# Performance work log

Measured on AMD Instinct MI355X. Metric: run time of the kernel, lower is better.

Reference implementation:

```python
import jax, jax.numpy as jnp
import numpy as np

B, N, INDIM, OUTDIM = 32, 128, 32, 64


def setup_inputs() -> dict:
    key = jax.random.key(0)
    k1, k2, k3, k4, k5, k6 = jax.random.split(key, 6)
    X = jax.random.normal(k1, (B, N, N, INDIM), dtype=jnp.float32)
    # variable subgraph sizes (irregular masking), at least 1 node per graph
    n_nodes = jnp.clip(jax.random.randint(k2, (B,), 0, N), 1, N).astype(jnp.int64)
    # MLP params (Linear + ReLU tail activation) for lin1 and lin2
    s = 1.0 / np.sqrt(INDIM)
    W1 = jax.random.uniform(k3, (INDIM, OUTDIM), jnp.float32, -s, s)
    b1 = jax.random.uniform(k4, (OUTDIM,), jnp.float32, -s, s)
    W2 = jax.random.uniform(k5, (INDIM, OUTDIM), jnp.float32, -s, s)
    b2 = jax.random.uniform(k6, (OUTDIM,), jnp.float32, -s, s)
    return {"X": X, "W1": W1, "b1": b1, "W2": W2, "b2": b2, "n_nodes": n_nodes}


def reference(X, W1, b1, W2, b2, n_nodes):
    # pairwise mask [B,N,N,1] from per-graph node counts (MaskedTensor mode 'DD')
    nm = jnp.arange(N)[None, :] < n_nodes[:, None]          # [B,N] node mask
    mask = (nm[:, :, None] & nm[:, None, :])[..., None].astype(X.dtype)  # [B,N,N,1]
    # tuplewiseapply of lin1 / lin2 (Linear + ReLU), zero-fill masked tuples
    X1 = jax.nn.relu(jnp.einsum('bijd,de->bije', X, W1) + b1) * mask  # [B,N,N,OUTDIM]
    X2 = jax.nn.relu(jnp.einsum('bijd,de->bije', X, W2) + b2) * mask
    # Op2FWL (aggr='sum'): per-channel batched matmul over node dim k
    out = jnp.einsum('bike,bkje->bije', X1, X2) * mask
    return out
```

## Files before the change

kernel.cpp:

```cpp
#include <hip/hip_runtime.h>

typedef unsigned short ushort_t;
typedef __attribute__((ext_vector_type(8))) __bf16 bf16x8;
typedef __attribute__((ext_vector_type(4))) float f32x4;


__device__ __forceinline__ ushort_t f32_to_bf16(float v) {
    unsigned ui = __float_as_uint(v);
    ui += 0x7fffu + ((ui >> 16) & 1u);
    return (ushort_t)(ui >> 16);
}

union FragU { bf16x8 f; ushort_t u[8]; };
union Pack4 { ushort_t us[4]; uint2 v; };

__global__ __launch_bounds__(256) void lin_mfma_kernel(
        const float* __restrict__ X,
        const float* __restrict__ W1, const float* __restrict__ b1v,
        const float* __restrict__ W2, const float* __restrict__ b2v,
        const int* __restrict__ n_nodes,
        ushort_t* __restrict__ X1t, ushort_t* __restrict__ X2t) {
    __shared__ ushort_t sO[64 * 136];
    const int blk = blockIdx.x;
    const int pass = blk >> 10;
    const int idx = blk & 1023;
    const int b = idx >> 5, rg = idx & 31;
    const int n = n_nodes[b];
    if (rg * 4 >= n) return;

    const float* W    = pass ? W2  : W1;
    const float* bias = pass ? b2v : b1v;
    ushort_t* Out     = pass ? X2t : X1t;
    const int rstride = pass ? 32 : 4096;
    const int tstride = pass ? 4096 : 32;

    const int u = threadIdx.x;
    const int w = u >> 6, l = u & 63;
    const int quad = l >> 4, lid = l & 15;

    FragU bfrag[4];
    float bia[4];
    #pragma unroll
    for (int ni = 0; ni < 4; ++ni) {
        const int e = ni * 16 + lid;
        #pragma unroll
        for (int j = 0; j < 8; ++j)
            bfrag[ni].u[j] = f32_to_bf16(W[(quad * 8 + j) * 64 + e]);
        bia[ni] = bias[e];
    }

    for (int q = 0; q < 4; ++q) {
        const int r = rg * 4 + q;
        if (r >= n) break;
        {
            const float* Xb = X + (size_t)b * 524288 + (size_t)r * rstride;
            #pragma unroll
            for (int s = 0; s < 2; ++s) {
                const int mt = w * 2 + s;
                const int t0b = mt * 16 + quad * 4;
                if (mt * 16 < n) {
                    const int m = mt * 16 + lid;
                    const float* xr = Xb + (size_t)m * tstride + quad * 8;
                    float4 x0 = *(const float4*)xr;
                    float4 x1 = *(const float4*)(xr + 4);
                    FragU af;
                    af.u[0] = f32_to_bf16(x0.x); af.u[1] = f32_to_bf16(x0.y);
                    af.u[2] = f32_to_bf16(x0.z); af.u[3] = f32_to_bf16(x0.w);
                    af.u[4] = f32_to_bf16(x1.x); af.u[5] = f32_to_bf16(x1.y);
                    af.u[6] = f32_to_bf16(x1.z); af.u[7] = f32_to_bf16(x1.w);
                    #pragma unroll
                    for (int ni = 0; ni < 4; ++ni) {
                        f32x4 acc = {};
                        acc = __builtin_amdgcn_mfma_f32_16x16x32_bf16(
                            af.f, bfrag[ni].f, acc, 0, 0, 0);
                        const int e = ni * 16 + lid;
                        Pack4 pk;
                        #pragma unroll
                        for (int rgi = 0; rgi < 4; ++rgi) {
                            const int t = t0b + rgi;
                            float v = (t < n) ? fmaxf(acc[rgi] + bia[ni], 0.f) : 0.f;
                            pk.us[rgi] = f32_to_bf16(v);
                        }
                        *(uint2*)(sO + e * 136 + t0b) = pk.v;
                    }
                } else {
                    Pack4 pk; pk.us[0] = pk.us[1] = pk.us[2] = pk.us[3] = 0;
                    #pragma unroll
                    for (int ni = 0; ni < 4; ++ni)
                        *(uint2*)(sO + (ni * 16 + lid) * 136 + t0b) = pk.v;
                }
            }
        }
        __syncthreads();
        {
            const int e = u >> 2, part = u & 3;
            if (part * 32 < n) {
                ushort_t* gO = Out + ((size_t)(b * 64 + e) * 128 + r) * 128 + part * 32;
                const ushort_t* sRow = sO + e * 136 + part * 32;
                #pragma unroll
                for (int c = 0; c < 4; ++c)
                    *(uint4*)(gO + c * 8) = *(const uint4*)(sRow + c * 8);
            }
        }
        __syncthreads();
    }
}

__global__ __launch_bounds__(256) void mmtr_kernel(
        const ushort_t* __restrict__ X1t, const ushort_t* __restrict__ X2t,
        float* __restrict__ out, const int* __restrict__ n_nodes) {
    __shared__ float sC[8 * 32 * 36];
    const int blk = blockIdx.x;
    const int b = blk >> 4, it = (blk >> 2) & 3, jt = blk & 3;
    const int i0 = it * 32, j0 = jt * 32;
    const int n = n_nodes[b];
    const int u = threadIdx.x;
    float* base = out + ((size_t)((b * 128 + i0) * 128 + j0)) * 64;

    if (i0 >= n || j0 >= n) {
        float4 z = {0.f, 0.f, 0.f, 0.f};
        for (int il = 0; il < 32; ++il) {
            float4* r = (float4*)(base + (size_t)il * 8192);
            r[u] = z; r[u + 256] = z;
        }
        return;
    }

    const int w = u >> 6, l = u & 63;
    const int quad = l >> 4, lid = l & 15;
    const int kmax = (n + 31) & ~31;
    const size_t pb = (size_t)(b * 64) * 16384;
    const ushort_t* Aj = X2t + pb;
    const ushort_t* Bi = X1t + pb;

    for (int g = 0; g < 8; ++g) {
        const int e0 = g * 8 + w * 2;
        const ushort_t* A0 = Aj + (size_t)e0 * 16384;
        const ushort_t* B0 = Bi + (size_t)e0 * 16384;
        const ushort_t* A1 = A0 + 16384;
        const ushort_t* B1 = B0 + 16384;
        f32x4 acc[2][2][2] = {};

        for (int k0 = 0; k0 < kmax; k0 += 32) {
            bf16x8 a0[2], a1[2], b0[2], b1[2];
            #pragma unroll
            for (int mj = 0; mj < 2; ++mj) {
                const size_t off = (size_t)(j0 + mj * 16 + lid) * 128 + k0 + quad * 8;
                a0[mj] = *(const bf16x8*)(A0 + off);
                a1[mj] = *(const bf16x8*)(A1 + off);
            }
            #pragma unroll
            for (int ni = 0; ni < 2; ++ni) {
                const size_t off = (size_t)(i0 + ni * 16 + lid) * 128 + k0 + quad * 8;
                b0[ni] = *(const bf16x8*)(B0 + off);
                b1[ni] = *(const bf16x8*)(B1 + off);
            }
            #pragma unroll
            for (int mj = 0; mj < 2; ++mj)
                #pragma unroll
                for (int ni = 0; ni < 2; ++ni) {
                    acc[0][mj][ni] = __builtin_amdgcn_mfma_f32_16x16x32_bf16(
                        a0[mj], b0[ni], acc[0][mj][ni], 0, 0, 0);
                    acc[1][mj][ni] = __builtin_amdgcn_mfma_f32_16x16x32_bf16(
                        a1[mj], b1[ni], acc[1][mj][ni], 0, 0, 0);
                }
        }

        #pragma unroll
        for (int ee = 0; ee < 2; ++ee) {
            const int el = w * 2 + ee;
            #pragma unroll
            for (int mj = 0; mj < 2; ++mj)
                #pragma unroll
                for (int ni = 0; ni < 2; ++ni) {
                    const int il = ni * 16 + lid;
                    const int jl = mj * 16 + quad * 4;
                    const bool iin = (i0 + il) < n;
                    float4 v;
                    v.x = (iin && (j0 + jl + 0) < n) ? acc[ee][mj][ni][0] : 0.f;
                    v.y = (iin && (j0 + jl + 1) < n) ? acc[ee][mj][ni][1] : 0.f;
                    v.z = (iin && (j0 + jl + 2) < n) ? acc[ee][mj][ni][2] : 0.f;
                    v.w = (iin && (j0 + jl + 3) < n) ? acc[ee][mj][ni][3] : 0.f;
                    *(float4*)(&sC[(el * 32 + il) * 36 + jl]) = v;
                }
        }
        __syncthreads();

        #pragma unroll
        for (int rep = 0; rep < 8; ++rep) {
            const int idx = rep * 256 + u;
            const int elq = idx & 1, jl = (idx >> 1) & 31, il = idx >> 6;
            float4 vv;
            vv.x = sC[((elq * 4 + 0) * 32 + il) * 36 + jl];
            vv.y = sC[((elq * 4 + 1) * 32 + il) * 36 + jl];
            vv.z = sC[((elq * 4 + 2) * 32 + il) * 36 + jl];
            vv.w = sC[((elq * 4 + 3) * 32 + il) * 36 + jl];
            *(float4*)(base + (size_t)il * 8192 + jl * 64 + g * 8 + elq * 4) = vv;
        }
        __syncthreads();
    }
}

extern "C" void kernel_launch(void* const* d_in, const int* in_sizes, int n_in,
                              void* d_out, int out_size, void* d_ws, size_t ws_size,
                              hipStream_t stream) {
    const float* X  = (const float*)d_in[0];
    const float* W1 = (const float*)d_in[1];
    const float* b1 = (const float*)d_in[2];
    const float* W2 = (const float*)d_in[3];
    const float* b2 = (const float*)d_in[4];
    const int* nn   = (const int*)d_in[5];
    float* out = (float*)d_out;

    ushort_t* X1t = (ushort_t*)d_ws;
    ushort_t* X2t = X1t + 33554432;

    lin_mfma_kernel<<<2048, 256, 0, stream>>>(X, W1, b1, W2, b2, nn, X1t, X2t);
    mmtr_kernel<<<512, 256, 0, stream>>>(X1t, X2t, out, nn);
}
```

Baseline: 317.5 us.

## Shrink output tiles to 16x16, stage all channels in LDS as bf16

The batched per-channel matmul kernel now uses 16x16 (i,j) tiles with four times as many blocks. Each wave computes 16 channels with a single MFMA per channel per k-step. All 64 channel results are staged in shared memory as bf16 and written out after a single barrier, instead of eight rounds of fp32 staging with two barriers each. This aims to raise parallelism and cut synchronisation. In exchange it loses operand reuse across sub-tiles and adds bf16 rounding of the final outputs.

```diff
diff --git a/kernel.cpp b/kernel.cpp
--- a/kernel.cpp
+++ b/kernel.cpp
@@ -106,23 +106,24 @@
     }
 }
 
-__global__ __launch_bounds__(256) void mmtr_kernel(
+#define JP 18
+#define EP 290
+__global__ __launch_bounds__(256) void mmo_kernel(
         const ushort_t* __restrict__ X1t, const ushort_t* __restrict__ X2t,
         float* __restrict__ out, const int* __restrict__ n_nodes) {
-    __shared__ float sC[8 * 32 * 36];
+    __shared__ ushort_t sC[64 * EP];
     const int blk = blockIdx.x;
-    const int b = blk >> 4, it = (blk >> 2) & 3, jt = blk & 3;
-    const int i0 = it * 32, j0 = jt * 32;
+    const int b = blk >> 6, it = (blk >> 3) & 7, jt = blk & 7;
+    const int i0 = it * 16, j0 = jt * 16;
     const int n = n_nodes[b];
     const int u = threadIdx.x;
     float* base = out + ((size_t)((b * 128 + i0) * 128 + j0)) * 64;
 
     if (i0 >= n || j0 >= n) {
         float4 z = {0.f, 0.f, 0.f, 0.f};
-        for (int il = 0; il < 32; ++il) {
-            float4* r = (float4*)(base + (size_t)il * 8192);
-            r[u] = z; r[u + 256] = z;
-        }
+        #pragma unroll
+        for (int il = 0; il < 16; ++il)
+            *((float4*)(base + (size_t)il * 8192) + u) = z;
         return;
     }
 
@@ -130,74 +131,58 @@
     const int quad = l >> 4, lid = l & 15;
     const int kmax = (n + 31) & ~31;
     const size_t pb = (size_t)(b * 64) * 16384;
-    const ushort_t* Aj = X2t + pb;
-    const ushort_t* Bi = X1t + pb;
-
-    for (int g = 0; g < 8; ++g) {
-        const int e0 = g * 8 + w * 2;
-        const ushort_t* A0 = Aj + (size_t)e0 * 16384;
-        const ushort_t* B0 = Bi + (size_t)e0 * 16384;
-        const ushort_t* A1 = A0 + 16384;
-        const ushort_t* B1 = B0 + 16384;
-        f32x4 acc[2][2][2] = {};
-
+    const bool iin = (i0 + lid) < n;
+
+    for (int g = 0; g < 4; ++g) {
+        const int e0 = w * 16 + g * 4;
+        const ushort_t* Ap[4];
+        const ushort_t* Bp[4];
+        #pragma unroll
+        for (int ee = 0; ee < 4; ++ee) {
+            const size_t ep = pb + (size_t)(e0 + ee) * 16384;
+            Ap[ee] = X2t + ep + (size_t)(j0 + lid) * 128 + quad * 8;
+            Bp[ee] = X1t + ep + (size_t)(i0 + lid) * 128 + quad * 8;
+        }
+        f32x4 acc[4] = {};
         for (int k0 = 0; k0 < kmax; k0 += 32) {
-            bf16x8 a0[2], a1[2], b0[2], b1[2];
-            #pragma unroll
-            for (int mj = 0; mj < 2; ++mj) {
-                const size_t off = (size_t)(j0 + mj * 16 + lid) * 128 + k0 + quad * 8;
-                a0[mj] = *(const bf16x8*)(A0 + off);
-                a1[mj] = *(const bf16x8*)(A1 + off);
-            }
-            #pragma unroll
-            for (int ni = 0; ni < 2; ++ni) {
-                const size_t off = (size_t)(i0 + ni * 16 + lid) * 128 + k0 + quad * 8;
-                b0[ni] = *(const bf16x8*)(B0 + off);
-                b1[ni] = *(const bf16x8*)(B1 + off);
-            }
-            #pragma unroll
-            for (int mj = 0; mj < 2; ++mj)
-                #pragma unroll
-                for (int ni = 0; ni < 2; ++ni) {
-                    acc[0][mj][ni] = __builtin_amdgcn_mfma_f32_16x16x32_bf16(
-                        a0[mj], b0[ni], acc[0][mj][ni], 0, 0, 0);
-                    acc[1][mj][ni] = __builtin_amdgcn_mfma_f32_16x16x32_bf16(
-                        a1[mj], b1[ni], acc[1][mj][ni], 0, 0, 0);
-                }
-        }
-
-        #pragma unroll
-        for (int ee = 0; ee < 2; ++ee) {
-            const int el = w * 2 + ee;
-            #pragma unroll
-            for (int mj = 0; mj < 2; ++mj)
-                #pragma unroll
-                for (int ni = 0; ni < 2; ++ni) {
-                    const int il = ni * 16 + lid;
-                    const int jl = mj * 16 + quad * 4;
-                    const bool iin = (i0 + il) < n;
-                    float4 v;
-                    v.x = (iin && (j0 + jl + 0) < n) ? acc[ee][mj][ni][0] : 0.f;
-                    v.y = (iin && (j0 + jl + 1) < n) ? acc[ee][mj][ni][1] : 0.f;
-                    v.z = (iin && (j0 + jl + 2) < n) ? acc[ee][mj][ni][2] : 0.f;
-                    v.w = (iin && (j0 + jl + 3) < n) ? acc[ee][mj][ni][3] : 0.f;
-                    *(float4*)(&sC[(el * 32 + il) * 36 + jl]) = v;
-                }
-        }
-        __syncthreads();
-
-        #pragma unroll
-        for (int rep = 0; rep < 8; ++rep) {
-            const int idx = rep * 256 + u;
-            const int elq = idx & 1, jl = (idx >> 1) & 31, il = idx >> 6;
-            float4 vv;
-            vv.x = sC[((elq * 4 + 0) * 32 + il) * 36 + jl];
-            vv.y = sC[((elq * 4 + 1) * 32 + il) * 36 + jl];
-            vv.z = sC[((elq * 4 + 2) * 32 + il) * 36 + jl];
-            vv.w = sC[((elq * 4 + 3) * 32 + il) * 36 + jl];
-            *(float4*)(base + (size_t)il * 8192 + jl * 64 + g * 8 + elq * 4) = vv;
-        }
-        __syncthreads();
+            bf16x8 af[4], bf[4];
+            #pragma unroll
+            for (int ee = 0; ee < 4; ++ee) {
+                af[ee] = *(const bf16x8*)(Ap[ee] + k0);
+                bf[ee] = *(const bf16x8*)(Bp[ee] + k0);
+            }
+            #pragma unroll
+            for (int ee = 0; ee < 4; ++ee)
+                acc[ee] = __builtin_amdgcn_mfma_f32_16x16x32_bf16(
+                    af[ee], bf[ee], acc[ee], 0, 0, 0);
+        }
+        #pragma unroll
+        for (int ee = 0; ee < 4; ++ee) {
+            Pack4 pk;
+            #pragma unroll
+            for (int rg = 0; rg < 4; ++rg) {
+                const int j = quad * 4 + rg;
+                float v = (iin && (j0 + j) < n) ? acc[ee][rg] : 0.f;
+                pk.us[rg] = f32_to_bf16(v);
+            }
+            ushort_t* s = sC + (e0 + ee) * EP + lid * JP + quad * 4;
+            *(unsigned*)(s)     = pk.v.x;
+            *(unsigned*)(s + 2) = pk.v.y;
+        }
+    }
+    __syncthreads();
+
+    const int e4 = u & 15, jl = u >> 4;
+    const ushort_t* s0 = sC + (e4 * 4) * EP + jl;
+    #pragma unroll
+    for (int il = 0; il < 16; ++il) {
+        const ushort_t* s = s0 + il * JP;
+        float4 vv;
+        vv.x = __uint_as_float((unsigned)s[0]      << 16);
+        vv.y = __uint_as_float((unsigned)s[EP]     << 16);
+        vv.z = __uint_as_float((unsigned)s[2 * EP] << 16);
+        vv.w = __uint_as_float((unsigned)s[3 * EP] << 16);
+        *(float4*)(base + (size_t)il * 8192 + jl * 64 + e4 * 4) = vv;
     }
 }
 
@@ -216,5 +201,5 @@
     ushort_t* X2t = X1t + 33554432;
 
     lin_mfma_kernel<<<2048, 256, 0, stream>>>(X, W1, b1, W2, b2, nn, X1t, X2t);
-    mmtr_kernel<<<512, 256, 0, stream>>>(X1t, X2t, out, nn);
-}
+    mmo_kernel<<<2048, 256, 0, stream>>>(X1t, X2t, out, nn);
+}
```

Measured after the change: 304.5 us. 4.1% less time.
